# Optimization experiments

Measured on AMD Instinct MI355X. Metric: run time of the kernel, lower is better.

Reference implementation:

```python
import jax, jax.numpy as jnp
import numpy as np

NUM_JOINT = 19
BATCH = 262144
ROOT_SCALE = 200.0
# Topologically-ordered humanoid skeleton: parent[j] < j for all non-root joints.
# 0: hips, 1-4: spine/head chain, 5-8: left arm, 9-12: right arm, 13-15: left leg, 16-18: right leg
PARENTS = np.array([-1, 0, 1, 2, 3, 2, 5, 6, 7, 2, 9, 10, 11, 0, 13, 14, 0, 16, 17], dtype=np.int32)


def quaternion_to_matrix(q):
    # q: [..., 4] in (w, x, y, z) order (pytorch3d convention, non-unit tolerant)
    w, x, y, z = q[..., 0], q[..., 1], q[..., 2], q[..., 3]
    two_s = 2.0 / jnp.sum(q * q, axis=-1)
    r = jnp.stack([
        1.0 - two_s * (y * y + z * z), two_s * (x * y - z * w), two_s * (x * z + y * w),
        two_s * (x * y + z * w), 1.0 - two_s * (x * x + z * z), two_s * (y * z - x * w),
        two_s * (x * z - y * w), two_s * (y * z + x * w), 1.0 - two_s * (x * x + y * y),
    ], axis=-1)
    return r.reshape(q.shape[:-1] + (3, 3))


def setup_inputs() -> dict:
    key = jax.random.key(0)
    k1, k2, k3 = jax.random.split(key, 3)
    root_position = jax.random.normal(k1, (BATCH, 3), dtype=jnp.float32)
    joint = jax.random.normal(k2, (BATCH, NUM_JOINT * 4), dtype=jnp.float32)
    # Homogeneous translation matrices per bone: identity rotation, translation in column 3.
    trans = jax.random.normal(k3, (NUM_JOINT, 3), dtype=jnp.float32) * 10.0
    offsets = jnp.tile(jnp.eye(4, dtype=jnp.float32)[None], (NUM_JOINT, 1, 1))
    offsets = offsets.at[:, :3, 3].set(trans)
    return {"root_position": root_position, "joint": joint, "offsets": offsets}


def reference(root_position, joint, offsets):
    B = joint.shape[0]
    q = joint.reshape(B, NUM_JOINT, 4)
    R3 = quaternion_to_matrix(q)  # [B, J, 3, 3]
    R4 = jnp.zeros((B, NUM_JOINT, 4, 4), dtype=joint.dtype)
    R4 = R4.at[:, :, :3, :3].set(R3).at[:, :, 3, 3].set(1.0)
    # RT = rotation @ bone offset, batched over all joints at once
    RT = jnp.einsum('bjik,jkl->bjil', R4, offsets)  # [B, J, 4, 4]
    # Sequential parent-child chain over the (small, fixed) skeleton tree
    mats = [RT[:, 0]]
    for j in range(1, NUM_JOINT):
        mats.append(jnp.matmul(mats[PARENTS[j]], RT[:, j]))
    M = jnp.stack(mats, axis=1)  # [B, J, 4, 4] world transforms
    # joint position = column 3 of the homogeneous transform (== transpose row 3 in source)
    pos = M[:, :, :, 3]  # [B, J, 4]
    pos = pos.at[:, :, :3].add((root_position * ROOT_SCALE)[:, None, :])
    return pos
```

## Files before the change

### kernel.cpp

```cpp
#include <hip/hip_runtime.h>

#define NJ 19
#define ROOT_SCALE 200.0f
#define BLOCK 128
#define ROWF 76
#define ROWV 19
#define STRIDE 84

struct Xform { float r[9]; float t[3]; };

__device__ __forceinline__ void quat_rt(float w, float x, float y, float z,
                                        float tx, float ty, float tz, Xform& o) {
    float ts = 2.0f / (w*w + x*x + y*y + z*z);
    o.r[0] = 1.0f - ts*(y*y + z*z); o.r[1] = ts*(x*y - z*w);        o.r[2] = ts*(x*z + y*w);
    o.r[3] = ts*(x*y + z*w);        o.r[4] = 1.0f - ts*(x*x + z*z); o.r[5] = ts*(y*z - x*w);
    o.r[6] = ts*(x*z - y*w);        o.r[7] = ts*(y*z + x*w);        o.r[8] = 1.0f - ts*(x*x + y*y);
    o.t[0] = o.r[0]*tx + o.r[1]*ty + o.r[2]*tz;
    o.t[1] = o.r[3]*tx + o.r[4]*ty + o.r[5]*tz;
    o.t[2] = o.r[6]*tx + o.r[7]*ty + o.r[8]*tz;
}

__device__ __forceinline__ void compose(const Xform& p, const Xform& l, Xform& o) {
#pragma unroll
    for (int i = 0; i < 3; ++i) {
        o.r[i*3+0] = p.r[i*3+0]*l.r[0] + p.r[i*3+1]*l.r[3] + p.r[i*3+2]*l.r[6];
        o.r[i*3+1] = p.r[i*3+0]*l.r[1] + p.r[i*3+1]*l.r[4] + p.r[i*3+2]*l.r[7];
        o.r[i*3+2] = p.r[i*3+0]*l.r[2] + p.r[i*3+1]*l.r[5] + p.r[i*3+2]*l.r[8];
        o.t[i]     = p.r[i*3+0]*l.t[0] + p.r[i*3+1]*l.t[1] + p.r[i*3+2]*l.t[2] + p.t[i];
    }
}

__global__ __launch_bounds__(BLOCK) void fk_kernel(
    const float* __restrict__ root, const float* __restrict__ joint,
    const float* __restrict__ offs, float* __restrict__ out, int batch)
{
    __shared__ float s[BLOCK * STRIDE];
    const int tid = threadIdx.x;
    const int rowBase = blockIdx.x * BLOCK;
    const long long gbase = (long long)rowBase * ROWF;
    const int nvalid = min(BLOCK, batch - rowBase);

    if (nvalid == BLOCK) {
#pragma unroll
        for (int i = 0; i < ROWV; ++i) {
            int v = i * BLOCK + tid;
            int r = v / ROWV;
            int c = (v - r * ROWV) * 4;
            float4 val = *(const float4*)(joint + gbase + (long long)v * 4);
            *(float4*)(&s[r * STRIDE + c]) = val;
        }
    } else {
        for (int v = tid; v < nvalid * ROWV; v += BLOCK) {
            int r = v / ROWV;
            int c = (v - r * ROWV) * 4;
            float4 val = *(const float4*)(joint + gbase + (long long)v * 4);
            *(float4*)(&s[r * STRIDE + c]) = val;
        }
    }
    __syncthreads();

    if (tid < nvalid) {
        float* row = &s[tid * STRIDE];
        const int b = rowBase + tid;
        const float rx = root[(long long)b*3 + 0] * ROOT_SCALE;
        const float ry = root[(long long)b*3 + 1] * ROOT_SCALE;
        const float rz = root[(long long)b*3 + 2] * ROOT_SCALE;

        Xform cur, sv0, sv2, loc;
#pragma unroll
        for (int j = 0; j < NJ; ++j) {
            float4 q = *(const float4*)(&row[j*4]);
            float tx = offs[j*16 + 3], ty = offs[j*16 + 7], tz = offs[j*16 + 11];
            quat_rt(q.x, q.y, q.z, q.w, tx, ty, tz, loc);
            if (j == 0) {
                cur = loc;
            } else {
                Xform nxt;
                if (j == 5 || j == 9)        compose(sv2, loc, nxt);
                else if (j == 13 || j == 16) compose(sv0, loc, nxt);
                else                         compose(cur, loc, nxt);
                cur = nxt;
            }
            if (j == 0) sv0 = cur;
            if (j == 2) sv2 = cur;
            float4 o;
            o.x = cur.t[0] + rx;
            o.y = cur.t[1] + ry;
            o.z = cur.t[2] + rz;
            o.w = 1.0f;
            *(float4*)(&row[j*4]) = o;
        }
    }
    __syncthreads();

    if (nvalid == BLOCK) {
#pragma unroll
        for (int i = 0; i < ROWV; ++i) {
            int v = i * BLOCK + tid;
            int r = v / ROWV;
            int c = (v - r * ROWV) * 4;
            *(float4*)(out + gbase + (long long)v * 4) = *(const float4*)(&s[r * STRIDE + c]);
        }
    } else {
        for (int v = tid; v < nvalid * ROWV; v += BLOCK) {
            int r = v / ROWV;
            int c = (v - r * ROWV) * 4;
            *(float4*)(out + gbase + (long long)v * 4) = *(const float4*)(&s[r * STRIDE + c]);
        }
    }
}

extern "C" void kernel_launch(void* const* d_in, const int* in_sizes, int n_in,
                              void* d_out, int out_size, void* d_ws, size_t ws_size,
                              hipStream_t stream) {
    const float* root  = (const float*)d_in[0];
    const float* joint = (const float*)d_in[1];
    const float* offs  = (const float*)d_in[2];
    float* out = (float*)d_out;
    const int batch = in_sizes[1] / ROWF;
    const int grid = (batch + BLOCK - 1) / BLOCK;
    fk_kernel<<<grid, BLOCK, 0, stream>>>(root, joint, offs, out, batch);
}
```

Before: 153.1 us.

## Drop shared-memory staging and load/store joint rows directly per thread

Removes the LDS transpose staging and both block barriers, so each thread reads its quaternions and writes its positions straight from and to global memory with float4 accesses. Block size grows from 128 to 256. This eliminates the 43KB shared allocation that limited occupancy and removes the synchronization, but makes global accesses strided per lane rather than coalesced, relying on caches to merge them.

```diff
diff --git a/kernel.cpp b/kernel.cpp
--- a/kernel.cpp
+++ b/kernel.cpp
@@ -2,10 +2,7 @@
 
 #define NJ 19
 #define ROOT_SCALE 200.0f
-#define BLOCK 128
-#define ROWF 76
-#define ROWV 19
-#define STRIDE 84
+#define BLOCK 256
 
 struct Xform { float r[9]; float t[3]; };
 
@@ -34,79 +31,39 @@
     const float* __restrict__ root, const float* __restrict__ joint,
     const float* __restrict__ offs, float* __restrict__ out, int batch)
 {
-    __shared__ float s[BLOCK * STRIDE];
-    const int tid = threadIdx.x;
-    const int rowBase = blockIdx.x * BLOCK;
-    const long long gbase = (long long)rowBase * ROWF;
-    const int nvalid = min(BLOCK, batch - rowBase);
+    const int b = blockIdx.x * BLOCK + threadIdx.x;
+    if (b >= batch) return;
 
-    if (nvalid == BLOCK) {
+    const float4* jq = (const float4*)joint + (long long)b * NJ;
+    float4*       op = (float4*)out        + (long long)b * NJ;
+
+    const float rx = root[(long long)b*3 + 0] * ROOT_SCALE;
+    const float ry = root[(long long)b*3 + 1] * ROOT_SCALE;
+    const float rz = root[(long long)b*3 + 2] * ROOT_SCALE;
+
+    Xform cur, sv0, sv2, loc;
 #pragma unroll
-        for (int i = 0; i < ROWV; ++i) {
-            int v = i * BLOCK + tid;
-            int r = v / ROWV;
-            int c = (v - r * ROWV) * 4;
-            float4 val = *(const float4*)(joint + gbase + (long long)v * 4);
-            *(float4*)(&s[r * STRIDE + c]) = val;
+    for (int j = 0; j < NJ; ++j) {
+        float4 q = jq[j];
+        float tx = offs[j*16 + 3], ty = offs[j*16 + 7], tz = offs[j*16 + 11];
+        quat_rt(q.x, q.y, q.z, q.w, tx, ty, tz, loc);
+        if (j == 0) {
+            cur = loc;
+        } else {
+            Xform nxt;
+            if (j == 5 || j == 9)        compose(sv2, loc, nxt);
+            else if (j == 13 || j == 16) compose(sv0, loc, nxt);
+            else                         compose(cur, loc, nxt);
+            cur = nxt;
         }
-    } else {
-        for (int v = tid; v < nvalid * ROWV; v += BLOCK) {
-            int r = v / ROWV;
-            int c = (v - r * ROWV) * 4;
-            float4 val = *(const float4*)(joint + gbase + (long long)v * 4);
-            *(float4*)(&s[r * STRIDE + c]) = val;
-        }
-    }
-    __syncthreads();
-
-    if (tid < nvalid) {
-        float* row = &s[tid * STRIDE];
-        const int b = rowBase + tid;
-        const float rx = root[(long long)b*3 + 0] * ROOT_SCALE;
-        const float ry = root[(long long)b*3 + 1] * ROOT_SCALE;
-        const float rz = root[(long long)b*3 + 2] * ROOT_SCALE;
-
-        Xform cur, sv0, sv2, loc;
-#pragma unroll
-        for (int j = 0; j < NJ; ++j) {
-            float4 q = *(const float4*)(&row[j*4]);
-            float tx = offs[j*16 + 3], ty = offs[j*16 + 7], tz = offs[j*16 + 11];
-            quat_rt(q.x, q.y, q.z, q.w, tx, ty, tz, loc);
-            if (j == 0) {
-                cur = loc;
-            } else {
-                Xform nxt;
-                if (j == 5 || j == 9)        compose(sv2, loc, nxt);
-                else if (j == 13 || j == 16) compose(sv0, loc, nxt);
-                else                         compose(cur, loc, nxt);
-                cur = nxt;
-            }
-            if (j == 0) sv0 = cur;
-            if (j == 2) sv2 = cur;
-            float4 o;
-            o.x = cur.t[0] + rx;
-            o.y = cur.t[1] + ry;
-            o.z = cur.t[2] + rz;
-            o.w = 1.0f;
-            *(float4*)(&row[j*4]) = o;
-        }
-    }
-    __syncthreads();
-
-    if (nvalid == BLOCK) {
-#pragma unroll
-        for (int i = 0; i < ROWV; ++i) {
-            int v = i * BLOCK + tid;
-            int r = v / ROWV;
-            int c = (v - r * ROWV) * 4;
-            *(float4*)(out + gbase + (long long)v * 4) = *(const float4*)(&s[r * STRIDE + c]);
-        }
-    } else {
-        for (int v = tid; v < nvalid * ROWV; v += BLOCK) {
-            int r = v / ROWV;
-            int c = (v - r * ROWV) * 4;
-            *(float4*)(out + gbase + (long long)v * 4) = *(const float4*)(&s[r * STRIDE + c]);
-        }
+        if (j == 0) sv0 = cur;
+        if (j == 2) sv2 = cur;
+        float4 o;
+        o.x = cur.t[0] + rx;
+        o.y = cur.t[1] + ry;
+        o.z = cur.t[2] + rz;
+        o.w = 1.0f;
+        op[j] = o;
     }
 }
 
@@ -117,7 +74,7 @@
     const float* joint = (const float*)d_in[1];
     const float* offs  = (const float*)d_in[2];
     float* out = (float*)d_out;
-    const int batch = in_sizes[1] / ROWF;
+    const int batch = in_sizes[1] / (NJ * 4);
     const int grid = (batch + BLOCK - 1) / BLOCK;
     fk_kernel<<<grid, BLOCK, 0, stream>>>(root, joint, offs, out, batch);
 }
```

New measurement: 258.2 us. 68.6% more time.
